# Performance work log

Measured on AMD Instinct MI355X. Metric: run time of the kernel, lower is better.

## Reference

```python
import jax, jax.numpy as jnp
import numpy as np

BS, CAMS, NQ, EMBED = 1, 6, 6400, 256
HEADS, LEVELS, POINTS, DEPTH = 8, 4, 8, 4
DH = EMBED // HEADS
SHAPES = np.array([[64, 176], [32, 88], [16, 44], [8, 22]], dtype=np.int64)  # (H, W) per level
FLEN = int((SHAPES[:, 0] * SHAPES[:, 1]).sum())  # 14960


def setup_inputs() -> dict:
    key = jax.random.key(0)
    ks = jax.random.split(key, 12)
    s = 0.02
    lsi = np.concatenate([[0], np.cumsum(SHAPES[:, 0] * SHAPES[:, 1])[:-1]]).astype(np.int64)
    return {
        'query': jax.random.normal(ks[0], (BS, NQ, EMBED), jnp.float32),
        'key': jax.random.normal(ks[1], (BS, FLEN, CAMS, EMBED), jnp.float32),
        'value': jax.random.normal(ks[2], (BS, FLEN, CAMS, EMBED), jnp.float32),
        'query_pos': jax.random.normal(ks[3], (BS, NQ, EMBED), jnp.float32),
        'reference_points_cam': jax.random.uniform(ks[4], (CAMS, BS, NQ, DEPTH, 2), jnp.float32),
        'bev_mask': jax.random.bernoulli(ks[5], 0.1, (CAMS, BS, NQ, DEPTH)),
        'spatial_shapes': jnp.asarray(SHAPES),
        'level_start_index': jnp.asarray(lsi),
        'Wv': jax.random.normal(ks[6], (EMBED, EMBED), jnp.float32) * s,
        'bv': jnp.zeros((EMBED,), jnp.float32),
        'Wso': jax.random.normal(ks[7], (EMBED, HEADS * LEVELS * POINTS * 2), jnp.float32) * s,
        'bso': jax.random.normal(ks[8], (HEADS * LEVELS * POINTS * 2,), jnp.float32) * s,
        'Waw': jax.random.normal(ks[9], (EMBED, HEADS * LEVELS * POINTS), jnp.float32) * s,
        'baw': jnp.zeros((HEADS * LEVELS * POINTS,), jnp.float32),
        'Wout': jax.random.normal(ks[10], (EMBED, EMBED), jnp.float32) * s,
        'bout': jnp.zeros((EMBED,), jnp.float32),
    }


def _bilinear_gather(v, xi, yi, Wl, Hl):
    # v: (B, Hl*Wl, H, Dh); xi, yi: (B, Nq, H, P) integer-valued floats.
    # grid_sample(padding_mode='zeros'): out-of-range corners contribute 0.
    valid = (xi >= 0) & (xi < Wl) & (yi >= 0) & (yi < Hl)
    idx = (jnp.clip(yi, 0, Hl - 1) * Wl + jnp.clip(xi, 0, Wl - 1)).astype(jnp.int32)
    B, Nq, Hh, P = idx.shape
    idx2 = idx.transpose(0, 1, 3, 2).reshape(B, Nq * P, Hh)[..., None]
    g = jnp.take_along_axis(v, idx2, axis=1)  # (B, Nq*P, Hh, Dh)
    g = g.reshape(B, Nq, P, Hh, -1).transpose(0, 1, 3, 2, 4)  # (B, Nq, Hh, P, Dh)
    return jnp.where(valid[..., None], g, 0.0)


def _msda(v, loc, aw):
    # Multi-scale deformable attn: v (B, Len, H, Dh); loc in [0,1] (B, Nq, H, L, P, 2); aw (B, Nq, H, L, P).
    out = 0.0
    start = 0
    for l in range(LEVELS):
        Hl, Wl = int(SHAPES[l, 0]), int(SHAPES[l, 1])
        vl = v[:, start:start + Hl * Wl]
        start += Hl * Wl
        # align_corners=False pixel coords
        x = loc[:, :, :, l, :, 0] * Wl - 0.5
        y = loc[:, :, :, l, :, 1] * Hl - 0.5
        x0 = jnp.floor(x)
        y0 = jnp.floor(y)
        wx1 = x - x0
        wy1 = y - y0
        s = (_bilinear_gather(vl, x0, y0, Wl, Hl) * ((1 - wx1) * (1 - wy1))[..., None]
             + _bilinear_gather(vl, x0 + 1, y0, Wl, Hl) * (wx1 * (1 - wy1))[..., None]
             + _bilinear_gather(vl, x0, y0 + 1, Wl, Hl) * ((1 - wx1) * wy1)[..., None]
             + _bilinear_gather(vl, x0 + 1, y0 + 1, Wl, Hl) * (wx1 * wy1)[..., None])
        out = out + jnp.einsum('bqhpd,bqhp->bqhd', s, aw[:, :, :, l])
    B, Nq = out.shape[0], out.shape[1]
    return out.reshape(B, Nq, -1)


def reference(query, key, value, query_pos, reference_points_cam, bev_mask,
              spatial_shapes, level_start_index, Wv, bv, Wso, bso, Waw, baw, Wout, bout):
    bs, nq, C = query.shape
    cams = bev_mask.shape[0]
    inp_residual = query  # residual is taken BEFORE query_pos is added
    q = query + query_pos
    # per-camera query visibility from batch-0 mask (as in the torch loop over bev_mask)
    mask_q = jnp.any(bev_mask[:, 0], axis=-1)  # (cams, nq)
    # instead of gather-rebatch to max_len, run attention for all queries and mask the scatter-add
    q_cam = jnp.broadcast_to(q[:, None], (bs, cams, nq, C)).reshape(bs * cams, nq, C)
    ref = jnp.transpose(reference_points_cam, (1, 0, 2, 3, 4)).reshape(bs * cams, nq, DEPTH, 2)
    v = jnp.transpose(value, (2, 0, 1, 3)).reshape(bs * cams, -1, C)
    # MSDeformableAttention3D (BEVFormer): value_proj, offsets, softmax weights, bilinear sampling
    v = (v @ Wv + bv).reshape(bs * cams, -1, HEADS, DH)
    off = (q_cam @ Wso + bso).reshape(bs * cams, nq, HEADS, LEVELS, POINTS, 2)
    norm = jnp.stack([spatial_shapes[:, 1], spatial_shapes[:, 0]], -1).astype(off.dtype)  # (L, 2) = (W, H)
    off = off / norm[None, None, None, :, None, :]
    aw = jax.nn.softmax((q_cam @ Waw + baw).reshape(bs * cams, nq, HEADS, LEVELS * POINTS), axis=-1)
    aw = aw.reshape(bs * cams, nq, HEADS, LEVELS, POINTS)
    pa = POINTS // DEPTH  # xy points per Z anchor
    loc = ref[:, :, None, None, None, :, :] + off.reshape(bs * cams, nq, HEADS, LEVELS, pa, DEPTH, 2)
    loc = loc.reshape(bs * cams, nq, HEADS, LEVELS, POINTS, 2)
    out = _msda(v, loc, aw).reshape(bs, cams, nq, C)
    # scatter-add back: slots[b, q] += sum_cam visible(cam, q) * out[b, cam, q]
    slots = jnp.sum(out * mask_q[None, :, :, None].astype(out.dtype), axis=1)
    count = jnp.any(bev_mask, axis=-1).transpose(1, 2, 0).sum(-1).astype(slots.dtype)  # (bs, nq)
    count = jnp.maximum(count, 1.0)
    slots = slots / count[..., None]
    slots = slots @ Wout + bout
    return slots + inp_residual  # dropout in eval mode = identity
```

## Files before the change

kernel.cpp:

```cpp
#include <hip/hip_runtime.h>
#include <hip/hip_bf16.h>

#define CAMS   6
#define NQ     6400
#define EMBED  256
#define HEADS  8
#define LEVELS 4
#define POINTS 8
#define DEPTH  4
#define DH     32
#define FLEN   14960
#define MV     (FLEN * CAMS)

__constant__ int c_LW[4] = {176, 88, 44, 22};
__constant__ int c_LH[4] = {64, 32, 16, 8};
__constant__ int c_LS[4] = {0, 11264, 14080, 14784};

typedef __bf16 bf16x8 __attribute__((ext_vector_type(8)));
typedef float  f32x4  __attribute__((ext_vector_type(4)));

__device__ __forceinline__ ushort f2bf(float x) {
    __hip_bfloat16 h = __float2bfloat16(x);
    return *(ushort*)&h;
}
__device__ __forceinline__ float bflo(unsigned u) { return __uint_as_float(u << 16); }
__device__ __forceinline__ float bfhi(unsigned u) { return __uint_as_float(u & 0xffff0000u); }

#define LSTRIDE 40

template <int MODE, int OUT>
__device__ __forceinline__ void gemm_body(ushort* sA, ushort* sB,
                                          const float* __restrict__ A,
                                          const float* __restrict__ A2,
                                          const float* __restrict__ W, int ldw,
                                          const float* __restrict__ bias,
                                          const float* __restrict__ resid,
                                          void* __restrict__ Cout, int ldc, int M,
                                          int bx, int by) {
    const int t = threadIdx.x;
    const int wave = t >> 6;
    const int lane = t & 63;
    const int wm = wave & 1, wn = wave >> 1;
    const int lane15 = lane & 15;
    const int laneq = lane >> 4;
    const int row0 = bx * 128;
    const int col0 = by * 128;

    f32x4 acc[4][4] = {};

    const int a_m = t >> 3;
    const int a_k = (t & 7) * 4;
    const int b_n = t & 127;
    const int b_k = (t >> 7) * 4;

    float4 aR[4], wR[4];

    #pragma unroll
    for (int p = 0; p < 4; ++p) {
        int gm = row0 + a_m + p * 32;
        if (gm >= M) gm = M - 1;
        aR[p] = *(const float4*)(A + (size_t)gm * 256 + a_k);
    }
    #pragma unroll
    for (int p = 0; p < 4; ++p) {
        const int k = b_k + p * 8;
        const float* wp = W + (size_t)k * ldw + col0 + b_n;
        wR[p] = make_float4(wp[0], wp[ldw], wp[2 * ldw], wp[3 * ldw]);
    }

    for (int k0 = 0; k0 < 256; k0 += 32) {
        #pragma unroll
        for (int p = 0; p < 4; ++p) {
            const int m = a_m + p * 32;
            float4 a4 = aR[p];
            if (MODE == 1) {
                int gm = row0 + m;
                if (gm >= M) gm = M - 1;
                float4 b4 = *(const float4*)(A2 + (size_t)gm * 256 + k0 + a_k);
                a4.x += b4.x; a4.y += b4.y; a4.z += b4.z; a4.w += b4.w;
            }
            *(ushort4*)(&sA[m * LSTRIDE + a_k]) =
                make_ushort4(f2bf(a4.x), f2bf(a4.y), f2bf(a4.z), f2bf(a4.w));
        }
        #pragma unroll
        for (int p = 0; p < 4; ++p) {
            const int k = b_k + p * 8;
            *(ushort4*)(&sB[b_n * LSTRIDE + k]) =
                make_ushort4(f2bf(wR[p].x), f2bf(wR[p].y), f2bf(wR[p].z), f2bf(wR[p].w));
        }
        __syncthreads();

        if (k0 + 32 < 256) {
            #pragma unroll
            for (int p = 0; p < 4; ++p) {
                int gm = row0 + a_m + p * 32;
                if (gm >= M) gm = M - 1;
                aR[p] = *(const float4*)(A + (size_t)gm * 256 + k0 + 32 + a_k);
            }
            #pragma unroll
            for (int p = 0; p < 4; ++p) {
                const int k = b_k + p * 8;
                const float* wp = W + (size_t)(k0 + 32 + k) * ldw + col0 + b_n;
                wR[p] = make_float4(wp[0], wp[ldw], wp[2 * ldw], wp[3 * ldw]);
            }
        }

        bf16x8 af[4], bfr[4];
        #pragma unroll
        for (int i = 0; i < 4; ++i) {
            const int m = wm * 64 + i * 16 + lane15;
            af[i] = *(const bf16x8*)(&sA[m * LSTRIDE + laneq * 8]);
            const int n = wn * 64 + i * 16 + lane15;
            bfr[i] = *(const bf16x8*)(&sB[n * LSTRIDE + laneq * 8]);
        }
        #pragma unroll
        for (int i = 0; i < 4; ++i)
            #pragma unroll
            for (int j = 0; j < 4; ++j)
                acc[i][j] = __builtin_amdgcn_mfma_f32_16x16x32_bf16(af[i], bfr[j], acc[i][j], 0, 0, 0);
        __syncthreads();
    }

    #pragma unroll
    for (int j = 0; j < 4; ++j) {
        const int col = col0 + wn * 64 + j * 16 + lane15;
        const float bcol = bias[col];
        #pragma unroll
        for (int i = 0; i < 4; ++i) {
            #pragma unroll
            for (int r = 0; r < 4; ++r) {
                const int row = row0 + wm * 64 + i * 16 + laneq * 4 + r;
                if (row < M) {
                    float v = acc[i][j][r] + bcol;
                    if (OUT == 1) {
                        const unsigned pix = ((unsigned)row * 43691u) >> 18;
                        const unsigned cam = (unsigned)row - pix * 6u;
                        const int hh = col >> 5, ch = col & 31;
                        ((ushort*)Cout)[((size_t)(cam * 8 + hh) * FLEN + pix) * 32 + ch] = f2bf(v);
                    } else {
                        if (MODE == 3) v += resid[(size_t)row * 256 + col];
                        ((float*)Cout)[(size_t)row * ldc + col] = v;
                    }
                }
            }
        }
    }
}

__launch_bounds__(256)
__global__ void fused_pre_gemm(const float* __restrict__ value,
                               const float* __restrict__ query,
                               const float* __restrict__ query_pos,
                               const float* __restrict__ Wv,  const float* __restrict__ bv,
                               const float* __restrict__ Wso, const float* __restrict__ bso,
                               const float* __restrict__ Waw, const float* __restrict__ baw,
                               const void* __restrict__ bm,
                               ushort* __restrict__ v_ws,
                               float* __restrict__ off_ws,
                               float* __restrict__ aw_ws,
                               int* __restrict__ flag) {
    __shared__ ushort sA[128 * LSTRIDE];
    __shared__ ushort sB[128 * LSTRIDE];
    const int bid = blockIdx.x;
    if (bid < 1404) {
        gemm_body<0, 1>(sA, sB, value, nullptr, Wv, 256, bv, nullptr,
                        v_ws, 256, MV, bid >> 1, bid & 1);
    } else if (bid < 1604) {
        const int r = bid - 1404;
        gemm_body<1, 0>(sA, sB, query, query_pos, Wso, 512, bso, nullptr,
                        off_ws, 512, NQ, r >> 2, r & 3);
    } else if (bid < 1704) {
        const int r = bid - 1604;
        gemm_body<1, 0>(sA, sB, query, query_pos, Waw, 256, baw, nullptr,
                        aw_ws, 256, NQ, r >> 1, r & 1);
    } else {
        const int t = threadIdx.x;
        const uint4* p4 = (const uint4*)bm;
        unsigned acc = 0;
        for (int i = t; i < (CAMS * NQ * DEPTH) / 16; i += 256) {
            const uint4 w = p4[i];
            acc |= w.x | w.y | w.z | w.w;
        }
        #pragma unroll
        for (int off = 32; off >= 1; off >>= 1) acc |= __shfl_xor(acc, off);
        unsigned* sred = (unsigned*)sA;
        if ((t & 63) == 0) sred[t >> 6] = acc;
        __syncthreads();
        if (t == 0) {
            const unsigned a = sred[0] | sred[1] | sred[2] | sred[3];
            flag[0] = (a & 0xFFFFFF00u) ? 1 : 0;
        }
    }
}

__launch_bounds__(256)
__global__ void gemm_out_kernel(const float* __restrict__ slots,
                                const float* __restrict__ Wout,
                                const float* __restrict__ bout,
                                const float* __restrict__ query,
                                float* __restrict__ out) {
    __shared__ ushort sA[128 * LSTRIDE];
    __shared__ ushort sB[128 * LSTRIDE];
    const int bid = blockIdx.x;
    gemm_body<3, 0>(sA, sB, slots, nullptr, Wout, 256, bout, query,
                    out, 256, NQ, bid >> 1, bid & 1);
}

__launch_bounds__(256)
__global__ void sample_kernel(const ushort* __restrict__ v,
                              const float* __restrict__ off_ws,
                              const float* __restrict__ aw_logit,
                              const float* __restrict__ rp,
                              const void* __restrict__ bm,
                              const int* __restrict__ flag,
                              float* __restrict__ slots) {
    const int q = blockIdx.x;
    const int t = threadIdx.x;
    const int h = t >> 5;
    const int e8 = (t >> 2) & 7;
    const int ch8 = (t & 3) * 8;
    const int l = e8 >> 1;
    const int ebase = h * 32 + e8 * 4;

    const int Wl = c_LW[l], Hl = c_LH[l], St = c_LS[l];
    const float fWl = (float)Wl, fHl = (float)Hl;

    const int fmt = *flag;
    int am = 0, cnt = 0;
    if (fmt == 1) {
        #pragma unroll
        for (int cam = 0; cam < CAMS; ++cam) {
            const unsigned w = ((const unsigned*)bm)[cam * NQ + q];
            const int a = (w != 0u);
            am |= a << cam;
            cnt += a;
        }
    } else {
        #pragma unroll
        for (int cam = 0; cam < CAMS; ++cam) {
            const int4 w = ((const int4*)bm)[cam * NQ + q];
            const int a = ((w.x | w.y | w.z | w.w) != 0);
            am |= a << cam;
            cnt += a;
        }
    }
    const float invq = 1.0f / (float)(cnt > 0 ? cnt : 1);

    const float4 lg = *(const float4*)(aw_logit + (size_t)q * 256 + ebase);
    float mx = fmaxf(fmaxf(lg.x, lg.y), fmaxf(lg.z, lg.w));
    mx = fmaxf(mx, __shfl_xor(mx, 4));
    mx = fmaxf(mx, __shfl_xor(mx, 8));
    mx = fmaxf(mx, __shfl_xor(mx, 16));
    const float e0 = expf(lg.x - mx), e1 = expf(lg.y - mx);
    const float e2 = expf(lg.z - mx), e3 = expf(lg.w - mx);
    float s = e0 + e1 + e2 + e3;
    s += __shfl_xor(s, 4);
    s += __shfl_xor(s, 8);
    s += __shfl_xor(s, 16);
    const float sc = invq / s;
    const float awv[4] = {e0 * sc, e1 * sc, e2 * sc, e3 * sc};

    const float* ofp = off_ws + (size_t)q * 512 + ebase * 2;
    const float4 o01 = *(const float4*)(ofp);
    const float4 o23 = *(const float4*)(ofp + 4);
    const float offx[4] = {o01.x, o01.z, o23.x, o23.z};
    const float offy[4] = {o01.y, o01.w, o23.y, o23.w};

    float acc[8] = {};

    for (int cam = 0; cam < CAMS; ++cam) {
        if (!((am >> cam) & 1)) continue;

        const int camhF = (cam * 8 + h) * FLEN + St;

        const float4 r01 = *(const float4*)(rp + (size_t)cam * (NQ * 8) + q * 8);
        const float4 r23 = *(const float4*)(rp + (size_t)cam * (NQ * 8) + q * 8 + 4);
        const float rx[4] = {r01.x, r01.z, r23.x, r23.z};
        const float ry[4] = {r01.y, r01.w, r23.y, r23.w};

        int   addr[16];
        float wgt[16];
        #pragma unroll
        for (int j = 0; j < 4; ++j) {
            const float x = fmaf(rx[j], fWl, offx[j]) - 0.5f;
            const float y = fmaf(ry[j], fHl, offy[j]) - 0.5f;
            const float x0f = floorf(x), y0f = floorf(y);
            const int x0 = (int)x0f, y0 = (int)y0f;
            const float fx = x - x0f, fy = y - y0f;
            const float wx0 = 1.f - fx, wy0 = 1.f - fy;
            #pragma unroll
            for (int c = 0; c < 4; ++c) {
                const int cx = x0 + (c & 1);
                const int cy = y0 + (c >> 1);
                const bool valid = ((unsigned)cx < (unsigned)Wl) & ((unsigned)cy < (unsigned)Hl);
                const int pixo = valid ? (cy * Wl + cx) : 0;
                addr[j * 4 + c] = ((camhF + pixo) << 5) + ch8;
                wgt[j * 4 + c] = valid
                    ? (((c & 1) ? fx : wx0) * ((c >> 1) ? fy : wy0) * awv[j])
                    : 0.f;
            }
        }
        #pragma unroll
        for (int i = 0; i < 16; ++i) {
            const uint4 u = *(const uint4*)(v + addr[i]);
            const float w = wgt[i];
            acc[0] = fmaf(w, bflo(u.x), acc[0]);
            acc[1] = fmaf(w, bfhi(u.x), acc[1]);
            acc[2] = fmaf(w, bflo(u.y), acc[2]);
            acc[3] = fmaf(w, bfhi(u.y), acc[3]);
            acc[4] = fmaf(w, bflo(u.z), acc[4]);
            acc[5] = fmaf(w, bfhi(u.z), acc[5]);
            acc[6] = fmaf(w, bflo(u.w), acc[6]);
            acc[7] = fmaf(w, bfhi(u.w), acc[7]);
        }
    }

    #pragma unroll
    for (int i = 0; i < 8; ++i) {
        acc[i] += __shfl_xor(acc[i], 4);
        acc[i] += __shfl_xor(acc[i], 8);
        acc[i] += __shfl_xor(acc[i], 16);
    }
    slots[(size_t)q * 256 + h * 32 + ch8 + e8] = acc[e8];
}

extern "C" void kernel_launch(void* const* d_in, const int* in_sizes, int n_in,
                              void* d_out, int out_size, void* d_ws, size_t ws_size,
                              hipStream_t stream) {
    const float* query     = (const float*)d_in[0];
    const float* value     = (const float*)d_in[2];
    const float* query_pos = (const float*)d_in[3];
    const float* refpts    = (const float*)d_in[4];
    const void*  bev_mask  = d_in[5];
    const float* Wv   = (const float*)d_in[8];
    const float* bv   = (const float*)d_in[9];
    const float* Wso  = (const float*)d_in[10];
    const float* bso  = (const float*)d_in[11];
    const float* Waw  = (const float*)d_in[12];
    const float* baw  = (const float*)d_in[13];
    const float* Wout = (const float*)d_in[14];
    const float* bout = (const float*)d_in[15];
    float* out = (float*)d_out;

    ushort* v_ws  = (ushort*)d_ws;
    float* off_ws = (float*)(v_ws + (size_t)MV * 256);
    float* aw_ws  = off_ws + (size_t)NQ * 512;
    float* slots  = aw_ws + (size_t)NQ * 256;
    int*   flag   = (int*)(slots + (size_t)NQ * 256);

    hipLaunchKernelGGL(fused_pre_gemm, dim3(1705), dim3(256), 0, stream,
                       value, query, query_pos, Wv, bv, Wso, bso, Waw, baw,
                       bev_mask, v_ws, off_ws, aw_ws, flag);

    hipLaunchKernelGGL(sample_kernel, dim3(NQ), dim3(256), 0, stream,
                       v_ws, off_ws, aw_ws, refpts, bev_mask, flag, slots);

    hipLaunchKernelGGL(gemm_out_kernel, dim3(100), dim3(256), 0, stream,
                       slots, Wout, bout, query, out);
}
```

Before: 367.6 us.

## Restructure value projection as persistent blocks with whole Wv resident in LDS

The value projection GEMM moves from 128x128 tiles that reload Wv slices to 256 persistent blocks. Each block converts the full 256x256 Wv to bf16 once into a 128KB swizzled LDS buffer, then loops over 32-row chunks, feeding A straight from global memory into MFMA. This removes repeated weight staging and per-k-tile syncs for the largest GEMM. In exchange, occupancy drops to one block per CU because of the large LDS allocation and launch_bounds(256,1), and that limit also applies to the smaller offset and attention-weight GEMM blocks sharing the kernel.

```diff
diff --git a/kernel.cpp b/kernel.cpp
--- a/kernel.cpp
+++ b/kernel.cpp
@@ -11,6 +11,7 @@
 #define DH     32
 #define FLEN   14960
 #define MV     (FLEN * CAMS)
+#define NCHUNK 2805
 
 __constant__ int c_LW[4] = {176, 88, 44, 22};
 __constant__ int c_LH[4] = {64, 32, 16, 8};
@@ -26,16 +27,23 @@
 __device__ __forceinline__ float bflo(unsigned u) { return __uint_as_float(u << 16); }
 __device__ __forceinline__ float bfhi(unsigned u) { return __uint_as_float(u & 0xffff0000u); }
 
+__device__ __forceinline__ bf16x8 pack8(float4 a, float4 b) {
+    union { ushort u[8]; bf16x8 v; } r;
+    r.u[0] = f2bf(a.x); r.u[1] = f2bf(a.y); r.u[2] = f2bf(a.z); r.u[3] = f2bf(a.w);
+    r.u[4] = f2bf(b.x); r.u[5] = f2bf(b.y); r.u[6] = f2bf(b.z); r.u[7] = f2bf(b.w);
+    return r.v;
+}
+
 #define LSTRIDE 40
 
-template <int MODE, int OUT>
+template <int MODE>
 __device__ __forceinline__ void gemm_body(ushort* sA, ushort* sB,
                                           const float* __restrict__ A,
                                           const float* __restrict__ A2,
                                           const float* __restrict__ W, int ldw,
                                           const float* __restrict__ bias,
                                           const float* __restrict__ resid,
-                                          void* __restrict__ Cout, int ldc, int M,
+                                          float* __restrict__ Cout, int ldc, int M,
                                           int bx, int by) {
     const int t = threadIdx.x;
     const int wave = t >> 6;
@@ -132,22 +140,95 @@
                 const int row = row0 + wm * 64 + i * 16 + laneq * 4 + r;
                 if (row < M) {
                     float v = acc[i][j][r] + bcol;
-                    if (OUT == 1) {
-                        const unsigned pix = ((unsigned)row * 43691u) >> 18;
-                        const unsigned cam = (unsigned)row - pix * 6u;
-                        const int hh = col >> 5, ch = col & 31;
-                        ((ushort*)Cout)[((size_t)(cam * 8 + hh) * FLEN + pix) * 32 + ch] = f2bf(v);
-                    } else {
-                        if (MODE == 3) v += resid[(size_t)row * 256 + col];
-                        ((float*)Cout)[(size_t)row * ldc + col] = v;
-                    }
+                    if (MODE == 3) v += resid[(size_t)row * 256 + col];
+                    Cout[(size_t)row * ldc + col] = v;
                 }
             }
         }
     }
 }
 
-__launch_bounds__(256)
+__device__ __forceinline__ void vproj_body(ushort* sW,
+                                           const float* __restrict__ A,
+                                           const float* __restrict__ W,
+                                           const float* __restrict__ bias,
+                                           ushort* __restrict__ v_ws,
+                                           int bid) {
+    const int t = threadIdx.x;
+
+    {
+        const int n = t;
+        const int xr = (n & 7) << 3;
+        #pragma unroll 8
+        for (int r = 0; r < 64; ++r) {
+            const int k4 = r * 4;
+            const float w0 = W[(size_t)(k4 + 0) * 256 + n];
+            const float w1 = W[(size_t)(k4 + 1) * 256 + n];
+            const float w2 = W[(size_t)(k4 + 2) * 256 + n];
+            const float w3 = W[(size_t)(k4 + 3) * 256 + n];
+            *(ushort4*)(&sW[n * 256 + (k4 ^ xr)]) =
+                make_ushort4(f2bf(w0), f2bf(w1), f2bf(w2), f2bf(w3));
+        }
+    }
+    __syncthreads();
+
+    const int wave = t >> 6, lane = t & 63;
+    const int lane15 = lane & 15, laneq = lane >> 4;
+
+    float bcol[16];
+    #pragma unroll
+    for (int nt = 0; nt < 16; ++nt) bcol[nt] = bias[nt * 16 + lane15];
+
+    const int g = bid * 4 + wave;
+    for (int c = g; c < NCHUNK; c += 1024) {
+        const int rowbase = c * 32;
+        const float* ap0 = A + (size_t)(rowbase + lane15) * 256 + laneq * 8;
+        const float* ap1 = ap0 + 16 * 256;
+
+        float4 a[2][8][2];
+        #pragma unroll
+        for (int s = 0; s < 8; ++s) {
+            a[0][s][0] = *(const float4*)(ap0 + s * 32);
+            a[0][s][1] = *(const float4*)(ap0 + s * 32 + 4);
+            a[1][s][0] = *(const float4*)(ap1 + s * 32);
+            a[1][s][1] = *(const float4*)(ap1 + s * 32 + 4);
+        }
+
+        f32x4 acc[2][16] = {};
+        #pragma unroll
+        for (int s = 0; s < 8; ++s) {
+            const bf16x8 fa0 = pack8(a[0][s][0], a[0][s][1]);
+            const bf16x8 fa1 = pack8(a[1][s][0], a[1][s][1]);
+            const int kb = laneq * 8 + s * 32;
+            #pragma unroll
+            for (int nt = 0; nt < 16; ++nt) {
+                const int n = nt * 16 + lane15;
+                const bf16x8 fb = *(const bf16x8*)(&sW[n * 256 + (kb ^ ((n & 7) << 3))]);
+                acc[0][nt] = __builtin_amdgcn_mfma_f32_16x16x32_bf16(fa0, fb, acc[0][nt], 0, 0, 0);
+                acc[1][nt] = __builtin_amdgcn_mfma_f32_16x16x32_bf16(fa1, fb, acc[1][nt], 0, 0, 0);
+            }
+        }
+
+        #pragma unroll
+        for (int rt = 0; rt < 2; ++rt) {
+            #pragma unroll
+            for (int r = 0; r < 4; ++r) {
+                const int row = rowbase + rt * 16 + laneq * 4 + r;
+                const unsigned pix = ((unsigned)row * 43691u) >> 18;
+                const unsigned cam = (unsigned)row - pix * 6u;
+                const unsigned base = (cam * 8u * FLEN + pix) * 32u;
+                #pragma unroll
+                for (int nt = 0; nt < 16; ++nt) {
+                    const unsigned idx = base + (unsigned)(nt >> 1) * (FLEN * 32u)
+                                       + (unsigned)((nt & 1) * 16 + lane15);
+                    v_ws[idx] = f2bf(acc[rt][nt][r] + bcol[nt]);
+                }
+            }
+        }
+    }
+}
+
+__launch_bounds__(256, 1)
 __global__ void fused_pre_gemm(const float* __restrict__ value,
                                const float* __restrict__ query,
                                const float* __restrict__ query_pos,
@@ -159,20 +240,18 @@
                                float* __restrict__ off_ws,
                                float* __restrict__ aw_ws,
                                int* __restrict__ flag) {
-    __shared__ ushort sA[128 * LSTRIDE];
-    __shared__ ushort sB[128 * LSTRIDE];
+    __shared__ ushort sW[256 * 256];
     const int bid = blockIdx.x;
-    if (bid < 1404) {
-        gemm_body<0, 1>(sA, sB, value, nullptr, Wv, 256, bv, nullptr,
-                        v_ws, 256, MV, bid >> 1, bid & 1);
-    } else if (bid < 1604) {
-        const int r = bid - 1404;
-        gemm_body<1, 0>(sA, sB, query, query_pos, Wso, 512, bso, nullptr,
-                        off_ws, 512, NQ, r >> 2, r & 3);
-    } else if (bid < 1704) {
-        const int r = bid - 1604;
-        gemm_body<1, 0>(sA, sB, query, query_pos, Waw, 256, baw, nullptr,
-                        aw_ws, 256, NQ, r >> 1, r & 1);
+    if (bid < 256) {
+        vproj_body(sW, value, Wv, bv, v_ws, bid);
+    } else if (bid < 456) {
+        const int r = bid - 256;
+        gemm_body<1>(sW, sW + 128 * LSTRIDE, query, query_pos, Wso, 512, bso, nullptr,
+                     off_ws, 512, NQ, r >> 2, r & 3);
+    } else if (bid < 556) {
+        const int r = bid - 456;
+        gemm_body<1>(sW, sW + 128 * LSTRIDE, query, query_pos, Waw, 256, baw, nullptr,
+                     aw_ws, 256, NQ, r >> 1, r & 1);
     } else {
         const int t = threadIdx.x;
         const uint4* p4 = (const uint4*)bm;
@@ -183,7 +262,7 @@
         }
         #pragma unroll
         for (int off = 32; off >= 1; off >>= 1) acc |= __shfl_xor(acc, off);
-        unsigned* sred = (unsigned*)sA;
+        unsigned* sred = (unsigned*)sW;
         if ((t & 63) == 0) sred[t >> 6] = acc;
         __syncthreads();
         if (t == 0) {
@@ -202,8 +281,8 @@
     __shared__ ushort sA[128 * LSTRIDE];
     __shared__ ushort sB[128 * LSTRIDE];
     const int bid = blockIdx.x;
-    gemm_body<3, 0>(sA, sB, slots, nullptr, Wout, 256, bout, query,
-                    out, 256, NQ, bid >> 1, bid & 1);
+    gemm_body<3>(sA, sB, slots, nullptr, Wout, 256, bout, query,
+                 out, 256, NQ, bid >> 1, bid & 1);
 }
 
 __launch_bounds__(256)
@@ -348,7 +427,7 @@
     float* slots  = aw_ws + (size_t)NQ * 256;
     int*   flag   = (int*)(slots + (size_t)NQ * 256);
 
-    hipLaunchKernelGGL(fused_pre_gemm, dim3(1705), dim3(256), 0, stream,
+    hipLaunchKernelGGL(fused_pre_gemm, dim3(557), dim3(256), 0, stream,
                        value, query, query_pos, Wv, bv, Wso, bso, Waw, baw,
                        bev_mask, v_ws, off_ws, aw_ws, flag);
 
```

After: 355.9 us. 1.03x faster.
